# Kernel optimization log

Hardware: AMD Instinct MI355X
Metric: run time of the kernel (lower is better)

Reference implementation:

```python
import jax, jax.numpy as jnp
import numpy as np

FP8_MAX = 448.0  # max finite value of float8_e4m3fn


def setup_inputs() -> dict:
    key = jax.random.key(0)
    k1, k2, k3 = jax.random.split(key, 3)
    B, S, D_IN, D_OUT = 2, 4096, 2048, 8192
    x = jax.random.normal(k1, (B, S, D_IN), dtype=jnp.float32)
    # Weight is stored pre-quantized in fp8 (per-tensor scale), layout (in, out)
    w_fp32 = jax.random.normal(k2, (D_IN, D_OUT), dtype=jnp.float32) * 0.02
    weight_scale = jnp.float32(jnp.max(jnp.abs(w_fp32)) / FP8_MAX)
    weight = jnp.clip(w_fp32 / weight_scale, -FP8_MAX, FP8_MAX).astype(jnp.float8_e4m3fn)
    input_scale = jnp.float32(0.05)  # static per-tensor activation scale
    bias = jax.random.normal(k3, (D_OUT,), dtype=jnp.float32)
    return {"x": x, "weight": weight, "weight_scale": weight_scale,
            "input_scale": input_scale, "bias": bias}


def reference(x, weight, weight_scale, input_scale, bias):
    # static_quantize_e4m3_per_tensor: q = cast_fp8(clip(x / s)), returns (q, s)
    q = jnp.clip(x / input_scale, -FP8_MAX, FP8_MAX).astype(jnp.float8_e4m3fn)
    q2d = q.reshape(-1, q.shape[-1]).astype(jnp.float32)  # [B*S, D_in]
    w = weight.astype(jnp.float32)                         # [D_in, D_out]
    # cublas_scaled_mm: (q @ w) * scale_a * scale_b, out in x.dtype
    out = jnp.matmul(q2d, w) * (input_scale * weight_scale)
    out = out.astype(x.dtype) + bias.astype(x.dtype)
    return out.reshape(x.shape[:-1] + (out.shape[-1],))
```

## Files before the change

kernel.cpp:

```cpp
#include <hip/hip_runtime.h>

typedef __attribute__((ext_vector_type(4))) float floatx4;
typedef __attribute__((ext_vector_type(8))) int   intx8;

__device__ __forceinline__ unsigned int pack4_fp8(float f0, float f1, float f2, float f3) {
    int v = __builtin_amdgcn_cvt_pk_fp8_f32(f0, f1, 0, false);
    v = __builtin_amdgcn_cvt_pk_fp8_f32(f2, f3, v, true);
    return (unsigned int)v;
}

__device__ __forceinline__ void gload16(const unsigned char* g, unsigned char* l) {
    __builtin_amdgcn_global_load_lds(
        (const __attribute__((address_space(1))) unsigned int*)g,
        (__attribute__((address_space(3))) unsigned int*)l, 16, 0, 0);
}

__global__ void detect_kernel(const unsigned int* __restrict__ W, int* __restrict__ flag) {
    __shared__ int ok[2];
    if (threadIdx.x == 0) { ok[0] = 1; ok[1] = 1; }
    __syncthreads();
    int f32ok = 1, bf16ok = 1;
#pragma unroll
    for (int i = 0; i < 16; ++i) {
        unsigned int w = W[threadIdx.x * 16 + i];
        if (w & 0x000FFFFFu) f32ok = 0;
        if (w & 0x000F000Fu) bf16ok = 0;
    }
    if (!f32ok)  atomicAnd(&ok[0], 0);
    if (!bf16ok) atomicAnd(&ok[1], 0);
    __syncthreads();
    if (threadIdx.x == 0) *flag = ok[0] ? 2 : (ok[1] ? 1 : 0);
}

__global__ void quant_kernel(const float* __restrict__ x,
                             unsigned int* __restrict__ q,
                             const float* __restrict__ iscale, int n8) {
    int i = blockIdx.x * blockDim.x + threadIdx.x;
    if (i >= n8) return;
    float s = iscale[0];
    const float4* xv = (const float4*)x;
    float4 a = xv[2 * i];
    float4 b = xv[2 * i + 1];
    float v[8] = {a.x, a.y, a.z, a.w, b.x, b.y, b.z, b.w};
#pragma unroll
    for (int j = 0; j < 8; ++j) {
        float t = v[j] / s;
        v[j] = fminf(fmaxf(t, -448.0f), 448.0f);
    }
    q[2 * i]     = pack4_fp8(v[0], v[1], v[2], v[3]);
    q[2 * i + 1] = pack4_fp8(v[4], v[5], v[6], v[7]);
}

template <int MODE>
__device__ __forceinline__ void ingest_body(const unsigned char* __restrict__ W,
                                            unsigned char* __restrict__ Wt,
                                            int K, int N,
                                            unsigned char (*tile)[68]) {
    const int k0 = blockIdx.y * 64;
    const int n0 = blockIdx.x * 64;
    const int t = threadIdx.x;
    const int kr = t >> 2;
    const int cg = (t & 3) * 16;
    const size_t eidx = (size_t)(k0 + kr) * N + (n0 + cg);

    unsigned int w4[4];
    if constexpr (MODE == 0) {
        uint4 v = *(const uint4*)(W + eidx);
        w4[0] = v.x; w4[1] = v.y; w4[2] = v.z; w4[3] = v.w;
    } else if constexpr (MODE == 1) {
        const uint4* p = (const uint4*)((const unsigned short*)W + eidx);
        uint4 A0 = p[0], A1 = p[1];
        unsigned int uw[8] = {A0.x, A0.y, A0.z, A0.w, A1.x, A1.y, A1.z, A1.w};
#pragma unroll
        for (int g = 0; g < 4; ++g) {
            float f0 = __uint_as_float((uw[2 * g] & 0xFFFFu) << 16);
            float f1 = __uint_as_float((uw[2 * g] >> 16) << 16);
            float f2 = __uint_as_float((uw[2 * g + 1] & 0xFFFFu) << 16);
            float f3 = __uint_as_float((uw[2 * g + 1] >> 16) << 16);
            w4[g] = pack4_fp8(f0, f1, f2, f3);
        }
    } else {
        const float4* p = (const float4*)((const float*)W + eidx);
#pragma unroll
        for (int g = 0; g < 4; ++g) {
            float4 f = p[g];
            w4[g] = pack4_fp8(f.x, f.y, f.z, f.w);
        }
    }
#pragma unroll
    for (int g = 0; g < 4; ++g)
        *(unsigned int*)&tile[kr][cg + 4 * g] = w4[g];
    __syncthreads();

    const int nr = t >> 2;
    const int kg = (t & 3) * 16;
    uint4 o;
    unsigned int w[4];
#pragma unroll
    for (int g = 0; g < 4; ++g) {
        unsigned int b0 = tile[kg + g * 4 + 0][nr];
        unsigned int b1 = tile[kg + g * 4 + 1][nr];
        unsigned int b2 = tile[kg + g * 4 + 2][nr];
        unsigned int b3 = tile[kg + g * 4 + 3][nr];
        w[g] = b0 | (b1 << 8) | (b2 << 16) | (b3 << 24);
    }
    o.x = w[0]; o.y = w[1]; o.z = w[2]; o.w = w[3];
    *(uint4*)(Wt + (size_t)(n0 + nr) * K + k0 + kg) = o;
}

__global__ void ingest_kernel(const unsigned char* __restrict__ W,
                              unsigned char* __restrict__ Wt,
                              const int* __restrict__ flag, int K, int N) {
    __shared__ __align__(16) unsigned char tile[64][68];
    const int mode = *flag;
    if (mode == 0)      ingest_body<0>(W, Wt, K, N, tile);
    else if (mode == 1) ingest_body<1>(W, Wt, K, N, tile);
    else                ingest_body<2>(W, Wt, K, N, tile);
}

__global__ __launch_bounds__(512, 2) void gemm_mxfp8_kernel(
    const unsigned char* __restrict__ A,
    const unsigned char* __restrict__ Bt,
    float* __restrict__ C,
    const float* __restrict__ bias,
    const float* __restrict__ wscale,
    const float* __restrict__ iscale,
    int M, int N, int K) {
    __shared__ __align__(16) unsigned char As[2][32768];
    __shared__ __align__(16) unsigned char Bs[2][32768];

    const int tid  = threadIdx.x;
    const int lane = tid & 63;
    const int wv   = tid >> 6;
    const int wm   = wv >> 2;
    const int wn   = wv & 3;
    const int r16  = lane & 15;
    const int cq   = lane >> 4;

    const int bm = blockIdx.y * 256;
    const int bn = blockIdx.x * 256;

    const unsigned char* ga[4];
    const unsigned char* gb[4];
    int lo[4];
#pragma unroll
    for (int j = 0; j < 4; ++j) {
        const int u   = wv * 4 + j;
        const int rb  = u >> 1;
        const int rg  = u & 1;
        const int row = rb * 16 + r16;
        const int col = cq * 32 + rg * 16;
        ga[j] = A  + (size_t)(bm + row) * K + col;
        gb[j] = Bt + (size_t)(bn + row) * K + col;
        lo[j] = u * 1024;
    }

    floatx4 acc[8][4] = {};

#pragma unroll
    for (int j = 0; j < 4; ++j) {
        gload16(ga[j], &As[0][lo[j]]);
        gload16(gb[j], &Bs[0][lo[j]]);
        ga[j] += 128; gb[j] += 128;
    }
    asm volatile("s_waitcnt vmcnt(0)" ::: "memory");
    __builtin_amdgcn_s_barrier();

    union U8 { intx8 v; uint4 q[2]; };
    const int NT = K >> 7;

#define READ_FRAG(dst, base, blk)                                   \
    do {                                                            \
        U8 _u;                                                      \
        const unsigned char* _p = (base) + (blk) * 2048 + lane * 16;\
        _u.q[0] = *(const uint4*)_p;                                \
        _u.q[1] = *(const uint4*)(_p + 1024);                       \
        (dst) = _u.v;                                               \
    } while (0)

#define MFMA8(a0, a1, i0, i1)                                               \
    do {                                                                    \
        __builtin_amdgcn_s_setprio(1);                                      \
        _Pragma("unroll")                                                   \
        for (int j = 0; j < 4; ++j)                                         \
            acc[i0][j] = __builtin_amdgcn_mfma_scale_f32_16x16x128_f8f6f4(  \
                a0, bf[j], acc[i0][j], 0, 0, 0, 0x7F7F7F7F, 0, 0x7F7F7F7F); \
        _Pragma("unroll")                                                   \
        for (int j = 0; j < 4; ++j)                                         \
            acc[i1][j] = __builtin_amdgcn_mfma_scale_f32_16x16x128_f8f6f4(  \
                a1, bf[j], acc[i1][j], 0, 0, 0, 0x7F7F7F7F, 0, 0x7F7F7F7F); \
        __builtin_amdgcn_s_setprio(0);                                      \
    } while (0)

#define PHASE_WAIT()                                             \
    do {                                                         \
        __builtin_amdgcn_s_barrier();                            \
        asm volatile("s_waitcnt lgkmcnt(0)" ::: "memory");       \
        __builtin_amdgcn_sched_barrier(0);                       \
    } while (0)

    for (int kt = 0; kt < NT; ++kt) {
        const unsigned char* Ab = As[kt & 1];
        const unsigned char* Bb = Bs[kt & 1];
        unsigned char* An = As[(kt & 1) ^ 1];
        unsigned char* Bn = Bs[(kt & 1) ^ 1];
        const bool pf = (kt + 1 < NT);

        intx8 bf[4], afa, afb;
        READ_FRAG(bf[0], Bb, wn * 4 + 0);
        READ_FRAG(bf[1], Bb, wn * 4 + 1);
        READ_FRAG(bf[2], Bb, wn * 4 + 2);
        READ_FRAG(bf[3], Bb, wn * 4 + 3);
        READ_FRAG(afa, Ab, wm * 8 + 0);
        READ_FRAG(afb, Ab, wm * 8 + 1);
        if (pf) {
            gload16(ga[0], An + lo[0]); gload16(ga[1], An + lo[1]);
            gload16(gb[0], Bn + lo[0]); gload16(gb[1], Bn + lo[1]);
            ga[0] += 128; ga[1] += 128; gb[0] += 128; gb[1] += 128;
        }
        PHASE_WAIT();
        MFMA8(afa, afb, 0, 1);
        __builtin_amdgcn_s_barrier();

        READ_FRAG(afa, Ab, wm * 8 + 2);
        READ_FRAG(afb, Ab, wm * 8 + 3);
        if (pf) {
            gload16(ga[2], An + lo[2]); gload16(ga[3], An + lo[3]);
            gload16(gb[2], Bn + lo[2]); gload16(gb[3], Bn + lo[3]);
            ga[2] += 128; ga[3] += 128; gb[2] += 128; gb[3] += 128;
        }
        PHASE_WAIT();
        MFMA8(afa, afb, 2, 3);
        __builtin_amdgcn_s_barrier();

        READ_FRAG(afa, Ab, wm * 8 + 4);
        READ_FRAG(afb, Ab, wm * 8 + 5);
        PHASE_WAIT();
        MFMA8(afa, afb, 4, 5);
        __builtin_amdgcn_s_barrier();

        READ_FRAG(afa, Ab, wm * 8 + 6);
        READ_FRAG(afb, Ab, wm * 8 + 7);
        PHASE_WAIT();
        MFMA8(afa, afb, 6, 7);
        asm volatile("s_waitcnt vmcnt(0)" ::: "memory");
        __builtin_amdgcn_s_barrier();
    }
    (void)M;
#undef READ_FRAG
#undef MFMA8
#undef PHASE_WAIT

    const float scale = iscale[0] * wscale[0];
    const int row0 = bm + wm * 128 + (cq << 2);
    const int col0 = bn + wn * 64 + r16;
#pragma unroll
    for (int j = 0; j < 4; ++j) {
        const int col = col0 + j * 16;
        const float bv = bias[col];
#pragma unroll
        for (int i = 0; i < 8; ++i) {
            const int row = row0 + i * 16;
            float* cp = C + (size_t)row * N + col;
#pragma unroll
            for (int r = 0; r < 4; ++r)
                cp[(size_t)r * N] = acc[i][j][r] * scale + bv;
        }
    }
}

extern "C" void kernel_launch(void* const* d_in, const int* in_sizes, int n_in,
                              void* d_out, int out_size, void* d_ws, size_t ws_size,
                              hipStream_t stream) {
    const float* x          = (const float*)d_in[0];
    const unsigned char* w  = (const unsigned char*)d_in[1];
    const float* wscale     = (const float*)d_in[2];
    const float* iscale     = (const float*)d_in[3];
    const float* bias       = (const float*)d_in[4];
    float* out              = (float*)d_out;

    const int D_OUT = in_sizes[4];
    const int D_IN  = in_sizes[1] / D_OUT;
    const int M     = in_sizes[0] / D_IN;

    int* flag         = (int*)d_ws;
    unsigned char* q  = (unsigned char*)d_ws + 256;
    unsigned char* wt = q + (size_t)M * D_IN;

    detect_kernel<<<1, 256, 0, stream>>>((const unsigned int*)w, flag);
    const int n8 = (M * D_IN) / 8;
    quant_kernel<<<(n8 + 255) / 256, 256, 0, stream>>>(x, (unsigned int*)q, iscale, n8);
    dim3 tg(D_OUT / 64, D_IN / 64);
    ingest_kernel<<<tg, 256, 0, stream>>>(w, wt, flag, D_IN, D_OUT);
    gemm_mxfp8_kernel<<<dim3(D_OUT / 256, M / 256), 512, 0, stream>>>(
        q, wt, out, bias, wscale, iscale, M, D_OUT, D_IN);
}
```

Baseline: 561.2 us.

## Prefetch B tiles two iterations ahead into the freed buffer

The A and B loads are now issued on separate schedules. A is still prefetched one k-tile ahead. B is prefetched two tiles ahead into the current B buffer, once all its fragments are already in registers. The end-of-iteration wait becomes vmcnt(4), so the B loads in flight carry across the barrier instead of draining every iteration. This is meant to hide more global-load latency. The cost is more complex wait-count bookkeeping, which depends on the compiler emitting no other vector memory ops.

Measured after the change: 549.8 us. 2.0% less time.

```diff
diff --git a/kernel.cpp b/kernel.cpp
--- a/kernel.cpp
+++ b/kernel.cpp
@@ -126,8 +126,8 @@
     const float* __restrict__ wscale,
     const float* __restrict__ iscale,
     int M, int N, int K) {
-    __shared__ __align__(16) unsigned char As[2][32768];
-    __shared__ __align__(16) unsigned char Bs[2][32768];
+    __shared__ __align__(16) unsigned char As[2 * 32768];
+    __shared__ __align__(16) unsigned char Bs[2 * 32768];
 
     const int tid  = threadIdx.x;
     const int lane = tid & 63;
@@ -156,18 +156,28 @@
     }
 
     floatx4 acc[8][4] = {};
+    const int NT = K >> 7;
 
 #pragma unroll
     for (int j = 0; j < 4; ++j) {
-        gload16(ga[j], &As[0][lo[j]]);
-        gload16(gb[j], &Bs[0][lo[j]]);
+        gload16(ga[j], &As[lo[j]]);
+        gload16(gb[j], &Bs[lo[j]]);
         ga[j] += 128; gb[j] += 128;
     }
-    asm volatile("s_waitcnt vmcnt(0)" ::: "memory");
+    if (NT > 1) {
+#pragma unroll
+        for (int j = 0; j < 4; ++j) {
+            gload16(gb[j], &Bs[32768 + lo[j]]);
+            gb[j] += 128;
+        }
+        asm volatile("s_waitcnt vmcnt(4)" ::: "memory");
+    } else {
+        asm volatile("s_waitcnt vmcnt(0)" ::: "memory");
+    }
     __builtin_amdgcn_s_barrier();
+    __builtin_amdgcn_sched_barrier(0);
 
     union U8 { intx8 v; uint4 q[2]; };
-    const int NT = K >> 7;
 
 #define READ_FRAG(dst, base, blk)                                   \
     do {                                                            \
@@ -200,11 +210,12 @@
     } while (0)
 
     for (int kt = 0; kt < NT; ++kt) {
-        const unsigned char* Ab = As[kt & 1];
-        const unsigned char* Bb = Bs[kt & 1];
-        unsigned char* An = As[(kt & 1) ^ 1];
-        unsigned char* Bn = Bs[(kt & 1) ^ 1];
-        const bool pf = (kt + 1 < NT);
+        const unsigned char* Ab = &As[(kt & 1) * 32768];
+        const unsigned char* Bb = &Bs[(kt & 1) * 32768];
+        unsigned char* An  = &As[((kt + 1) & 1) * 32768];
+        unsigned char* Bn2 = &Bs[(kt & 1) * 32768];
+        const bool pfA = (kt + 1 < NT);
+        const bool pfB = (kt + 2 < NT);
 
         intx8 bf[4], afa, afb;
         READ_FRAG(bf[0], Bb, wn * 4 + 0);
@@ -213,10 +224,9 @@
         READ_FRAG(bf[3], Bb, wn * 4 + 3);
         READ_FRAG(afa, Ab, wm * 8 + 0);
         READ_FRAG(afb, Ab, wm * 8 + 1);
-        if (pf) {
+        if (pfA) {
             gload16(ga[0], An + lo[0]); gload16(ga[1], An + lo[1]);
-            gload16(gb[0], Bn + lo[0]); gload16(gb[1], Bn + lo[1]);
-            ga[0] += 128; ga[1] += 128; gb[0] += 128; gb[1] += 128;
+            ga[0] += 128; ga[1] += 128;
         }
         PHASE_WAIT();
         MFMA8(afa, afb, 0, 1);
@@ -224,10 +234,9 @@
 
         READ_FRAG(afa, Ab, wm * 8 + 2);
         READ_FRAG(afb, Ab, wm * 8 + 3);
-        if (pf) {
+        if (pfA) {
             gload16(ga[2], An + lo[2]); gload16(ga[3], An + lo[3]);
-            gload16(gb[2], Bn + lo[2]); gload16(gb[3], Bn + lo[3]);
-            ga[2] += 128; ga[3] += 128; gb[2] += 128; gb[3] += 128;
+            ga[2] += 128; ga[3] += 128;
         }
         PHASE_WAIT();
         MFMA8(afa, afb, 2, 3);
@@ -235,16 +244,29 @@
 
         READ_FRAG(afa, Ab, wm * 8 + 4);
         READ_FRAG(afb, Ab, wm * 8 + 5);
+        if (pfB) {
+            gload16(gb[0], Bn2 + lo[0]); gload16(gb[1], Bn2 + lo[1]);
+            gb[0] += 128; gb[1] += 128;
+        }
         PHASE_WAIT();
         MFMA8(afa, afb, 4, 5);
         __builtin_amdgcn_s_barrier();
 
         READ_FRAG(afa, Ab, wm * 8 + 6);
         READ_FRAG(afb, Ab, wm * 8 + 7);
+        if (pfB) {
+            gload16(gb[2], Bn2 + lo[2]); gload16(gb[3], Bn2 + lo[3]);
+            gb[2] += 128; gb[3] += 128;
+        }
         PHASE_WAIT();
         MFMA8(afa, afb, 6, 7);
-        asm volatile("s_waitcnt vmcnt(0)" ::: "memory");
+        if (pfB) {
+            asm volatile("s_waitcnt vmcnt(4)" ::: "memory");
+        } else {
+            asm volatile("s_waitcnt vmcnt(0)" ::: "memory");
+        }
         __builtin_amdgcn_s_barrier();
+        __builtin_amdgcn_sched_barrier(0);
     }
     (void)M;
 #undef READ_FRAG
```

## Restructure GEMM main loop into two half-phases with upfront prefetch

Applied to the files above, without the earlier changes.

Replaces the four-phase k-loop (each phase with its own barrier and LDS wait) with two phases of sixteen MFMAs each. All global-to-LDS prefetches for the next tile are issued at the top of the iteration, and the second half of the A fragments is read from LDS while the first sixteen MFMAs run. The aim is fewer barriers per iteration and better overlap of LDS reads with matrix math. In exchange it holds more A fragment registers live, which may raise register pressure under the 512x2 launch bounds, and it drops the s_setprio priority hints.

Result: no change. 571.8 us (+1.9%).

```diff
diff --git a/kernel.cpp b/kernel.cpp
--- a/kernel.cpp
+++ b/kernel.cpp
@@ -126,8 +126,8 @@
     const float* __restrict__ wscale,
     const float* __restrict__ iscale,
     int M, int N, int K) {
-    __shared__ __align__(16) unsigned char As[2][32768];
-    __shared__ __align__(16) unsigned char Bs[2][32768];
+    __shared__ __align__(16) unsigned char As[2 * 32768];
+    __shared__ __align__(16) unsigned char Bs[2 * 32768];
 
     const int tid  = threadIdx.x;
     const int lane = tid & 63;
@@ -156,18 +156,19 @@
     }
 
     floatx4 acc[8][4] = {};
+    const int NT = K >> 7;
 
 #pragma unroll
     for (int j = 0; j < 4; ++j) {
-        gload16(ga[j], &As[0][lo[j]]);
-        gload16(gb[j], &Bs[0][lo[j]]);
+        gload16(ga[j], &As[lo[j]]);
+        gload16(gb[j], &Bs[lo[j]]);
         ga[j] += 128; gb[j] += 128;
     }
     asm volatile("s_waitcnt vmcnt(0)" ::: "memory");
     __builtin_amdgcn_s_barrier();
+    __builtin_amdgcn_sched_barrier(0);
 
     union U8 { intx8 v; uint4 q[2]; };
-    const int NT = K >> 7;
 
 #define READ_FRAG(dst, base, blk)                                   \
     do {                                                            \
@@ -178,78 +179,66 @@
         (dst) = _u.v;                                               \
     } while (0)
 
-#define MFMA8(a0, a1, i0, i1)                                               \
+#define MFMA16(af_, ibase)                                                  \
     do {                                                                    \
-        __builtin_amdgcn_s_setprio(1);                                      \
         _Pragma("unroll")                                                   \
-        for (int j = 0; j < 4; ++j)                                         \
-            acc[i0][j] = __builtin_amdgcn_mfma_scale_f32_16x16x128_f8f6f4(  \
-                a0, bf[j], acc[i0][j], 0, 0, 0, 0x7F7F7F7F, 0, 0x7F7F7F7F); \
-        _Pragma("unroll")                                                   \
-        for (int j = 0; j < 4; ++j)                                         \
-            acc[i1][j] = __builtin_amdgcn_mfma_scale_f32_16x16x128_f8f6f4(  \
-                a1, bf[j], acc[i1][j], 0, 0, 0, 0x7F7F7F7F, 0, 0x7F7F7F7F); \
-        __builtin_amdgcn_s_setprio(0);                                      \
+        for (int i = 0; i < 4; ++i)                                         \
+            _Pragma("unroll")                                               \
+            for (int j = 0; j < 4; ++j)                                     \
+                acc[(ibase) + i][j] =                                       \
+                    __builtin_amdgcn_mfma_scale_f32_16x16x128_f8f6f4(       \
+                        af_[i], bf[j], acc[(ibase) + i][j],                 \
+                        0, 0, 0, 0x7F7F7F7F, 0, 0x7F7F7F7F);                \
     } while (0)
 
-#define PHASE_WAIT()                                             \
-    do {                                                         \
-        __builtin_amdgcn_s_barrier();                            \
-        asm volatile("s_waitcnt lgkmcnt(0)" ::: "memory");       \
-        __builtin_amdgcn_sched_barrier(0);                       \
-    } while (0)
-
     for (int kt = 0; kt < NT; ++kt) {
-        const unsigned char* Ab = As[kt & 1];
-        const unsigned char* Bb = Bs[kt & 1];
-        unsigned char* An = As[(kt & 1) ^ 1];
-        unsigned char* Bn = Bs[(kt & 1) ^ 1];
-        const bool pf = (kt + 1 < NT);
-
-        intx8 bf[4], afa, afb;
+        const unsigned char* Ab = &As[(kt & 1) * 32768];
+        const unsigned char* Bb = &Bs[(kt & 1) * 32768];
+        unsigned char* An = &As[((kt + 1) & 1) * 32768];
+        unsigned char* Bn = &Bs[((kt + 1) & 1) * 32768];
+
+        if (kt + 1 < NT) {
+#pragma unroll
+            for (int j = 0; j < 4; ++j) {
+                gload16(ga[j], An + lo[j]);
+                gload16(gb[j], Bn + lo[j]);
+                ga[j] += 128; gb[j] += 128;
+            }
+        }
+
+        intx8 bf[4], af1[4], af2[4];
         READ_FRAG(bf[0], Bb, wn * 4 + 0);
         READ_FRAG(bf[1], Bb, wn * 4 + 1);
         READ_FRAG(bf[2], Bb, wn * 4 + 2);
         READ_FRAG(bf[3], Bb, wn * 4 + 3);
-        READ_FRAG(afa, Ab, wm * 8 + 0);
-        READ_FRAG(afb, Ab, wm * 8 + 1);
-        if (pf) {
-            gload16(ga[0], An + lo[0]); gload16(ga[1], An + lo[1]);
-            gload16(gb[0], Bn + lo[0]); gload16(gb[1], Bn + lo[1]);
-            ga[0] += 128; ga[1] += 128; gb[0] += 128; gb[1] += 128;
-        }
-        PHASE_WAIT();
-        MFMA8(afa, afb, 0, 1);
+        READ_FRAG(af1[0], Ab, wm * 8 + 0);
+        READ_FRAG(af1[1], Ab, wm * 8 + 1);
+        READ_FRAG(af1[2], Ab, wm * 8 + 2);
+        READ_FRAG(af1[3], Ab, wm * 8 + 3);
+
         __builtin_amdgcn_s_barrier();
-
-        READ_FRAG(afa, Ab, wm * 8 + 2);
-        READ_FRAG(afb, Ab, wm * 8 + 3);
-        if (pf) {
-            gload16(ga[2], An + lo[2]); gload16(ga[3], An + lo[3]);
-            gload16(gb[2], Bn + lo[2]); gload16(gb[3], Bn + lo[3]);
-            ga[2] += 128; ga[3] += 128; gb[2] += 128; gb[3] += 128;
-        }
-        PHASE_WAIT();
-        MFMA8(afa, afb, 2, 3);
-        __builtin_amdgcn_s_barrier();
-
-        READ_FRAG(afa, Ab, wm * 8 + 4);
-        READ_FRAG(afb, Ab, wm * 8 + 5);
-        PHASE_WAIT();
-        MFMA8(afa, afb, 4, 5);
-        __builtin_amdgcn_s_barrier();
-
-        READ_FRAG(afa, Ab, wm * 8 + 6);
-        READ_FRAG(afb, Ab, wm * 8 + 7);
-        PHASE_WAIT();
-        MFMA8(afa, afb, 6, 7);
+        asm volatile("s_waitcnt lgkmcnt(0)" ::: "memory");
+        __builtin_amdgcn_sched_barrier(0);
+
+        READ_FRAG(af2[0], Ab, wm * 8 + 4);
+        READ_FRAG(af2[1], Ab, wm * 8 + 5);
+        READ_FRAG(af2[2], Ab, wm * 8 + 6);
+        READ_FRAG(af2[3], Ab, wm * 8 + 7);
+
+        MFMA16(af1, 0);
+
+        asm volatile("s_waitcnt lgkmcnt(0)" ::: "memory");
+        __builtin_amdgcn_sched_barrier(0);
+
+        MFMA16(af2, 4);
+
         asm volatile("s_waitcnt vmcnt(0)" ::: "memory");
         __builtin_amdgcn_s_barrier();
+        __builtin_amdgcn_sched_barrier(0);
     }
     (void)M;
 #undef READ_FRAG
-#undef MFMA8
-#undef PHASE_WAIT
+#undef MFMA16
 
     const float scale = iscale[0] * wscale[0];
     const int row0 = bm + wm * 128 + (cq << 2);
```
